# Performance work log

Measured on AMD Instinct MI355X. Metric: run time of the kernel, lower is better.

Reference implementation:

```python
import jax, jax.numpy as jnp
import numpy as np

HID = 64

def _rnn_layer(x, W_ih, W_hh, b_ih, b_hh):
    # x: [B, T, F]; PyTorch RNN step: h_t = tanh(x_t @ W_ih.T + b_ih + h_{t-1} @ W_hh.T + b_hh)
    # Precompute the input projection for all timesteps as one big GEMM.
    x_proj = jnp.einsum('btf,hf->bth', x, W_ih) + b_ih  # [B, T, H]
    B = x.shape[0]
    h0 = jnp.zeros((B, HID), x.dtype)

    def step(h, xt):
        h = jnp.tanh(xt + h @ W_hh.T + b_hh)
        return h, h

    _, hs = jax.lax.scan(step, h0, jnp.swapaxes(x_proj, 0, 1))  # hs: [T, B, H]
    return jnp.swapaxes(hs, 0, 1)  # [B, T, H]


def setup_inputs() -> dict:
    key = jax.random.key(0)
    ks = jax.random.split(key, 20)
    B, T, F = 4096, 128, 14
    s_in = 1.0 / np.sqrt(HID)  # PyTorch RNN init scale
    d = {
        'x': jax.random.normal(ks[0], (B, T, F), jnp.float32),
        'W_ih0': jax.random.normal(ks[1], (HID, F), jnp.float32) * s_in,
        'W_hh0': jax.random.normal(ks[2], (HID, HID), jnp.float32) * s_in,
        'b_ih0': jax.random.normal(ks[3], (HID,), jnp.float32) * s_in,
        'b_hh0': jax.random.normal(ks[4], (HID,), jnp.float32) * s_in,
        'W_ih1': jax.random.normal(ks[5], (HID, HID), jnp.float32) * s_in,
        'W_hh1': jax.random.normal(ks[6], (HID, HID), jnp.float32) * s_in,
        'b_ih1': jax.random.normal(ks[7], (HID,), jnp.float32) * s_in,
        'b_hh1': jax.random.normal(ks[8], (HID,), jnp.float32) * s_in,
        'W_ih2': jax.random.normal(ks[9], (HID, HID), jnp.float32) * s_in,
        'W_hh2': jax.random.normal(ks[10], (HID, HID), jnp.float32) * s_in,
        'b_ih2': jax.random.normal(ks[11], (HID,), jnp.float32) * s_in,
        'b_hh2': jax.random.normal(ks[12], (HID,), jnp.float32) * s_in,
        'fc1_w': jax.random.normal(ks[13], (32, HID), jnp.float32) * s_in,
        'fc1_b': jax.random.normal(ks[14], (32,), jnp.float32) * s_in,
        'fc2_w': jax.random.normal(ks[15], (1, 32), jnp.float32) * (1.0 / np.sqrt(32)),
        'fc2_b': jax.random.normal(ks[16], (1,), jnp.float32) * (1.0 / np.sqrt(32)),
    }
    return d


def reference(x, W_ih0, W_hh0, b_ih0, b_hh0, W_ih1, W_hh1, b_ih1, b_hh1,
              W_ih2, W_hh2, b_ih2, b_hh2, fc1_w, fc1_b, fc2_w, fc2_b):
    h = _rnn_layer(x, W_ih0, W_hh0, b_ih0, b_hh0)
    h = _rnn_layer(h, W_ih1, W_hh1, b_ih1, b_hh1)
    h = _rnn_layer(h, W_ih2, W_hh2, b_ih2, b_hh2)
    last = h[:, -1, :]                       # [B, H]
    y = jax.nn.relu(last @ fc1_w.T + fc1_b)  # [B, 32]
    return y @ fc2_w.T + fc2_b               # [B, 1]
```

## Files before the change

### kernel.cpp

```cpp
#include <hip/hip_runtime.h>

typedef short  s16x8 __attribute__((ext_vector_type(8)));
typedef float  f32x4 __attribute__((ext_vector_type(4)));
typedef float  f32x2 __attribute__((ext_vector_type(2)));
typedef unsigned int u32;
typedef unsigned int u32x4 __attribute__((ext_vector_type(4)));
typedef unsigned short u16;

#define DEVI static __device__ __forceinline__

#if __has_builtin(__builtin_amdgcn_exp2f)
#define EXP2(v) __builtin_amdgcn_exp2f(v)
#else
#define EXP2(v) exp2f(v)
#endif

constexpr int T_  = 128;
constexpr int F_  = 14;
constexpr int H_  = 64;
constexpr int BPB = 16;
constexpr int K_  = 8;
constexpr int NCH = T_ / K_;

DEVI u16 f2bf(float f) {
  u32 u = __builtin_bit_cast(u32, f);
  u += 0x7fffu + ((u >> 16) & 1u);
  return (u16)(u >> 16);
}
DEVI u16 f2bfF(float f) {
  u32 u = __builtin_bit_cast(u32, f);
  return (u16)((u + 0x8000u) >> 16);
}
DEVI u32 pkbf(float a, float b) {
  u32 ua = __builtin_bit_cast(u32, a) + 0x8000u;
  u32 ub = __builtin_bit_cast(u32, b) + 0x8000u;
  return (ua >> 16) | (ub & 0xffff0000u);
}
DEVI s16x8 packfrag(const f32x4& a, const f32x4& b) {
  u32x4 p;
  p[0] = pkbf(a[0], a[1]); p[1] = pkbf(a[2], a[3]);
  p[2] = pkbf(b[0], b[1]); p[3] = pkbf(b[2], b[3]);
  return __builtin_bit_cast(s16x8, p);
}
DEVI float tanhfast(float x) {
  float e = EXP2(x * -2.8853900817779268f);
  float r = __builtin_amdgcn_rcpf(1.0f + e);
  return __builtin_fmaf(2.0f, r, -1.0f);
}
DEVI f32x4 tanh4(const f32x4& v) {
  f32x4 r;
  r[0] = tanhfast(v[0]); r[1] = tanhfast(v[1]);
  r[2] = tanhfast(v[2]); r[3] = tanhfast(v[3]);
  return r;
}
DEVI f32x4 MFMA(s16x8 a, s16x8 b, f32x4 c) {
  return __builtin_amdgcn_mfma_f32_16x16x32_bf16(a, b, c, 0, 0, 0);
}
DEVI s16x8 ldrow8(const float* p) {
  const f32x4 a = ((const f32x4*)p)[0];
  const f32x4 b = ((const f32x4*)p)[1];
  s16x8 r;
  r[0] = (short)f2bf(a[0]); r[1] = (short)f2bf(a[1]);
  r[2] = (short)f2bf(a[2]); r[3] = (short)f2bf(a[3]);
  r[4] = (short)f2bf(b[0]); r[5] = (short)f2bf(b[1]);
  r[6] = (short)f2bf(b[2]); r[7] = (short)f2bf(b[3]);
  return r;
}

__global__ __launch_bounds__(192, 1) void rnn_ck(
    const float* __restrict__ x,
    const float* __restrict__ Wih0, const float* __restrict__ Whh0,
    const float* __restrict__ bih0, const float* __restrict__ bhh0,
    const float* __restrict__ Wih1, const float* __restrict__ Whh1,
    const float* __restrict__ bih1, const float* __restrict__ bhh1,
    const float* __restrict__ Wih2, const float* __restrict__ Whh2,
    const float* __restrict__ bih2, const float* __restrict__ bhh2,
    const float* __restrict__ fc1w, const float* __restrict__ fc1b,
    const float* __restrict__ fc2w, const float* __restrict__ fc2b,
    float* __restrict__ out)
{
  __shared__ __align__(16) u32x4 hf[2][2][K_][2][64];

  const int tid  = threadIdx.x;
  const int w    = tid >> 6;
  const int lane = tid & 63;
  const int g    = lane >> 4;
  const int m    = lane & 15;
  const int b0   = blockIdx.x * BPB;

  f32x4 z4; z4[0] = 0.f; z4[1] = 0.f; z4[2] = 0.f; z4[3] = 0.f;

  s16x8 Ax[4], Ai[4][2], Ah[4][2];
  f32x4 bc[4];
  {
    const float* Wi = Wih1; const float* Wh = Whh0;
    const float* bi = bih0; const float* bh = bhh0;
    if (w == 1)      { Wi = Wih1; Wh = Whh1; bi = bih1; bh = bhh1; }
    else if (w == 2) { Wi = Wih2; Wh = Whh2; bi = bih2; bh = bhh2; }
    #pragma unroll
    for (int n = 0; n < 4; n++) {
      const int Lr = 32 * (n & 1) + 8 * (m >> 2) + 4 * (n >> 1) + (m & 3);
      if (w == 0) {
        s16x8 r;
        #pragma unroll
        for (int j2 = 0; j2 < 8; j2++) {
          const int kk = 8 * g + j2;
          r[j2] = (kk < F_) ? (short)f2bf(Wih0[Lr * F_ + kk]) : (short)0;
        }
        Ax[n] = r;
        Ai[n][0] = r; Ai[n][1] = r;
      } else {
        #pragma unroll
        for (int kt = 0; kt < 2; kt++)
          Ai[n][kt] = ldrow8(Wi + Lr * H_ + 32 * kt + 8 * g);
        Ax[n] = Ai[n][0];
      }
      #pragma unroll
      for (int kt = 0; kt < 2; kt++)
        Ah[n][kt] = ldrow8(Wh + Lr * H_ + 32 * kt + 8 * g);
      const int Lb = 32 * (n & 1) + 8 * g + 4 * (n >> 1);
      bc[n] = *(const f32x4*)(bi + Lb) + *(const f32x4*)(bh + Lb);
    }
  }

  s16x8 F[2];
  {
    s16x8 z;
    #pragma unroll
    for (int i = 0; i < 8; i++) z[i] = 0;
    F[0] = z; F[1] = z;
  }
  f32x4 h2v[4];
  #pragma unroll
  for (int n = 0; n < 4; n++) h2v[n] = z4;

  const float* xrow = x + (size_t)(b0 + m) * T_ * F_;
  auto ldraw = [&](int t, f32x4& ra, f32x4& rb) {
    const float* p = xrow + t * F_;
    if (g == 0) {
      f32x2 p0 = *(const f32x2*)(p),     p1 = *(const f32x2*)(p + 2);
      f32x2 p2 = *(const f32x2*)(p + 4), p3 = *(const f32x2*)(p + 6);
      ra[0] = p0[0]; ra[1] = p0[1]; ra[2] = p1[0]; ra[3] = p1[1];
      rb[0] = p2[0]; rb[1] = p2[1]; rb[2] = p3[0]; rb[3] = p3[1];
    } else if (g == 1) {
      f32x2 p4 = *(const f32x2*)(p + 8), p5 = *(const f32x2*)(p + 10);
      f32x2 p6 = *(const f32x2*)(p + 12);
      ra[0] = p4[0]; ra[1] = p4[1]; ra[2] = p5[0]; ra[3] = p5[1];
      rb[0] = p6[0]; rb[1] = p6[1]; rb[2] = 0.f;   rb[3] = 0.f;
    } else {
      ra = z4; rb = z4;
    }
  };
  auto cvtraw = [&](const f32x4& ra, const f32x4& rb) -> s16x8 {
    s16x8 r;
    r[0] = (short)f2bfF(ra[0]); r[1] = (short)f2bfF(ra[1]);
    r[2] = (short)f2bfF(ra[2]); r[3] = (short)f2bfF(ra[3]);
    r[4] = (short)f2bfF(rb[0]); r[5] = (short)f2bfF(rb[1]);
    r[6] = (short)f2bfF(rb[2]); r[7] = (short)f2bfF(rb[3]);
    return r;
  };

  s16x8 cur[K_];
  f32x4 nra[K_], nrb[K_];
  if (w == 0) {
    #pragma unroll
    for (int k = 0; k < K_; k++) { ldraw(k, nra[k], nrb[k]); }
    #pragma unroll
    for (int k = 0; k < K_; k++) cur[k] = cvtraw(nra[k], nrb[k]);
  }

  #pragma unroll 1
  for (int e = 0; e < NCH + 2; e++) {
    const int c  = e - w;
    const int wb = e & 1, rb = wb ^ 1;

    if (w == 0) {
      int cn = e + 1; if (cn > NCH - 1) cn = NCH - 1;
      #pragma unroll
      for (int k = 0; k < K_; k++) ldraw(cn * K_ + k, nra[k], nrb[k]);
    }

    if (c >= 0 && c < NCH) {
      #pragma unroll
      for (int k = 0; k < K_; k++) {
        s16x8 Fp0, Fp1;
        if (w == 0) {
          Fp0 = cur[k]; Fp1 = cur[k];
        } else if (w == 1) {
          Fp0 = __builtin_bit_cast(s16x8, hf[rb][0][k][0][lane]);
          Fp1 = __builtin_bit_cast(s16x8, hf[rb][0][k][1][lane]);
        } else {
          Fp0 = __builtin_bit_cast(s16x8, hf[rb][1][k][0][lane]);
          Fp1 = __builtin_bit_cast(s16x8, hf[rb][1][k][1][lane]);
        }
        f32x4 p[4], q[4], hv[4];
        #pragma unroll
        for (int n = 0; n < 4; n++) p[n] = MFMA(Ah[n][0], F[0], bc[n]);
        #pragma unroll
        for (int n = 0; n < 4; n++) p[n] = MFMA(Ah[n][1], F[1], p[n]);
        if (w == 0) {
          #pragma unroll
          for (int n = 0; n < 4; n++) q[n] = MFMA(Ax[n], Fp0, z4);
        } else {
          #pragma unroll
          for (int n = 0; n < 4; n++) q[n] = MFMA(Ai[n][0], Fp0, z4);
          #pragma unroll
          for (int n = 0; n < 4; n++) q[n] = MFMA(Ai[n][1], Fp1, q[n]);
        }
        #pragma unroll
        for (int n = 0; n < 4; n++) hv[n] = tanh4(p[n] + q[n]);
        F[0] = packfrag(hv[0], hv[2]);
        F[1] = packfrag(hv[1], hv[3]);
        if (w < 2) {
          hf[wb][w][k][0][lane] = __builtin_bit_cast(u32x4, F[0]);
          hf[wb][w][k][1][lane] = __builtin_bit_cast(u32x4, F[1]);
        } else if (c == NCH - 1 && k == K_ - 1) {
          #pragma unroll
          for (int n = 0; n < 4; n++) h2v[n] = hv[n];
        }
      }
    }

    if (w == 0) {
      #pragma unroll
      for (int k = 0; k < K_; k++) cur[k] = cvtraw(nra[k], nrb[k]);
    }
    __syncthreads();
  }

  float (*h2l)[68] = (float (*)[68])&hf[0][0][0][0][0];
  if (w == 2) {
    #pragma unroll
    for (int n = 0; n < 4; n++) {
      const int Lb = 32 * (n & 1) + 8 * g + 4 * (n >> 1);
      *(f32x4*)&h2l[m][Lb] = h2v[n];
    }
  }
  __syncthreads();

  if (w == 0) {
    float hr[64];
    #pragma unroll
    for (int q = 0; q < 16; q++) {
      f32x4 v = *(const f32x4*)&h2l[m][4 * q];
      hr[4 * q + 0] = v[0]; hr[4 * q + 1] = v[1];
      hr[4 * q + 2] = v[2]; hr[4 * q + 3] = v[3];
    }
    float acc2 = 0.f;
    #pragma unroll
    for (int jj = 0; jj < 8; jj++) {
      const int jf = 8 * g + jj;
      float s = fc1b[jf];
      const f32x4* wp = (const f32x4*)(fc1w + jf * H_);
      #pragma unroll
      for (int kq = 0; kq < 16; kq++) {
        f32x4 wv = wp[kq];
        s += hr[4 * kq + 0] * wv[0] + hr[4 * kq + 1] * wv[1]
           + hr[4 * kq + 2] * wv[2] + hr[4 * kq + 3] * wv[3];
      }
      s = fmaxf(s, 0.f);
      acc2 += s * fc2w[jf];
    }
    acc2 += __shfl_xor(acc2, 16, 64);
    acc2 += __shfl_xor(acc2, 32, 64);
    if (lane < 16) out[b0 + m] = acc2 + fc2b[0];
  }
}

extern "C" void kernel_launch(void* const* d_in, const int* in_sizes, int n_in,
                              void* d_out, int out_size, void* d_ws, size_t ws_size,
                              hipStream_t stream) {
  const float* x    = (const float*)d_in[0];
  const float* Wih0 = (const float*)d_in[1];
  const float* Whh0 = (const float*)d_in[2];
  const float* bih0 = (const float*)d_in[3];
  const float* bhh0 = (const float*)d_in[4];
  const float* Wih1 = (const float*)d_in[5];
  const float* Whh1 = (const float*)d_in[6];
  const float* bih1 = (const float*)d_in[7];
  const float* bhh1 = (const float*)d_in[8];
  const float* Wih2 = (const float*)d_in[9];
  const float* Whh2 = (const float*)d_in[10];
  const float* bih2 = (const float*)d_in[11];
  const float* bhh2 = (const float*)d_in[12];
  const float* fc1w = (const float*)d_in[13];
  const float* fc1b = (const float*)d_in[14];
  const float* fc2w = (const float*)d_in[15];
  const float* fc2b = (const float*)d_in[16];

  rnn_ck<<<dim3(4096 / BPB), dim3(192), 0, stream>>>(
      x, Wih0, Whh0, bih0, bhh0, Wih1, Whh1, bih1, bhh1,
      Wih2, Whh2, bih2, bhh2, fc1w, fc1b, fc2w, fc2b, (float*)d_out);
}
```

Before: 191.8 us.

## Software-pipeline input projection MFMAs and split x prefetch into half-chunks

Restructures the per-timestep loop so the input-projection MFMAs for step k+1 are issued during step k, taking them off the serial recurrence chain. The two recurrent MFMA halves are computed into independent accumulators and summed afterwards, which shortens the dependent MFMA chain. Layer-0 x prefetch is split into two groups of four timesteps interleaved within the chunk, reducing live registers compared with holding eight raw rows. The cost is extra register pressure from the qc/qn buffers and more complex scheduling.

```diff
diff --git a/kernel.cpp b/kernel.cpp
--- a/kernel.cpp
+++ b/kernel.cpp
@@ -67,7 +67,7 @@
   return r;
 }
 
-__global__ __launch_bounds__(192, 1) void rnn_ck(
+__global__ __launch_bounds__(192, 1) void rnn_sp(
     const float* __restrict__ x,
     const float* __restrict__ Wih0, const float* __restrict__ Whh0,
     const float* __restrict__ bih0, const float* __restrict__ bhh0,
@@ -161,54 +161,81 @@
   };
 
   s16x8 cur[K_];
-  f32x4 nra[K_], nrb[K_];
+  f32x4 ra4[4], rb4[4];
   if (w == 0) {
     #pragma unroll
-    for (int k = 0; k < K_; k++) { ldraw(k, nra[k], nrb[k]); }
-    #pragma unroll
-    for (int k = 0; k < K_; k++) cur[k] = cvtraw(nra[k], nrb[k]);
+    for (int k = 0; k < 4; k++) ldraw(k, ra4[k], rb4[k]);
+    #pragma unroll
+    for (int k = 0; k < 4; k++) cur[k] = cvtraw(ra4[k], rb4[k]);
+    #pragma unroll
+    for (int k = 0; k < 4; k++) ldraw(4 + k, ra4[k], rb4[k]);
+    #pragma unroll
+    for (int k = 0; k < 4; k++) cur[4 + k] = cvtraw(ra4[k], rb4[k]);
+    #pragma unroll
+    for (int k = 0; k < 4; k++) ldraw(K_ + k, ra4[k], rb4[k]);
   }
 
   #pragma unroll 1
   for (int e = 0; e < NCH + 2; e++) {
     const int c  = e - w;
-    const int wb = e & 1, rb = wb ^ 1;
-
-    if (w == 0) {
-      int cn = e + 1; if (cn > NCH - 1) cn = NCH - 1;
-      #pragma unroll
-      for (int k = 0; k < K_; k++) ldraw(cn * K_ + k, nra[k], nrb[k]);
-    }
+    const int wb = e & 1, rbuf = wb ^ 1;
 
     if (c >= 0 && c < NCH) {
+      const int cn = (c + 1 < NCH) ? c + 1 : NCH - 1;
+
+      s16x8 Fpc0, Fpc1, Fpn0, Fpn1;
+      if (w == 1) {
+        Fpc0 = __builtin_bit_cast(s16x8, hf[rbuf][0][0][0][lane]);
+        Fpc1 = __builtin_bit_cast(s16x8, hf[rbuf][0][0][1][lane]);
+      } else if (w == 2) {
+        Fpc0 = __builtin_bit_cast(s16x8, hf[rbuf][1][0][0][lane]);
+        Fpc1 = __builtin_bit_cast(s16x8, hf[rbuf][1][0][1][lane]);
+      } else {
+        Fpc0 = cur[0]; Fpc1 = cur[0];
+      }
+      f32x4 qc[4], qn[4];
+      if (w == 0) {
+        #pragma unroll
+        for (int n = 0; n < 4; n++) qc[n] = MFMA(Ax[n], Fpc0, z4);
+      } else {
+        #pragma unroll
+        for (int n = 0; n < 4; n++) qc[n] = MFMA(Ai[n][0], Fpc0, z4);
+        #pragma unroll
+        for (int n = 0; n < 4; n++) qc[n] = MFMA(Ai[n][1], Fpc1, qc[n]);
+      }
+
       #pragma unroll
       for (int k = 0; k < K_; k++) {
-        s16x8 Fp0, Fp1;
-        if (w == 0) {
-          Fp0 = cur[k]; Fp1 = cur[k];
-        } else if (w == 1) {
-          Fp0 = __builtin_bit_cast(s16x8, hf[rb][0][k][0][lane]);
-          Fp1 = __builtin_bit_cast(s16x8, hf[rb][0][k][1][lane]);
-        } else {
-          Fp0 = __builtin_bit_cast(s16x8, hf[rb][1][k][0][lane]);
-          Fp1 = __builtin_bit_cast(s16x8, hf[rb][1][k][1][lane]);
+        f32x4 pA[4], pB[4];
+        #pragma unroll
+        for (int n = 0; n < 4; n++) pA[n] = MFMA(Ah[n][0], F[0], bc[n]);
+        #pragma unroll
+        for (int n = 0; n < 4; n++) pB[n] = MFMA(Ah[n][1], F[1], z4);
+
+        if (k + 1 < K_) {
+          if (w == 1) {
+            Fpn0 = __builtin_bit_cast(s16x8, hf[rbuf][0][k + 1][0][lane]);
+            Fpn1 = __builtin_bit_cast(s16x8, hf[rbuf][0][k + 1][1][lane]);
+          } else if (w == 2) {
+            Fpn0 = __builtin_bit_cast(s16x8, hf[rbuf][1][k + 1][0][lane]);
+            Fpn1 = __builtin_bit_cast(s16x8, hf[rbuf][1][k + 1][1][lane]);
+          } else {
+            Fpn0 = cur[k + 1]; Fpn1 = cur[k + 1];
+          }
+          if (w == 0) {
+            #pragma unroll
+            for (int n = 0; n < 4; n++) qn[n] = MFMA(Ax[n], Fpn0, z4);
+          } else {
+            #pragma unroll
+            for (int n = 0; n < 4; n++) qn[n] = MFMA(Ai[n][0], Fpn0, z4);
+            #pragma unroll
+            for (int n = 0; n < 4; n++) qn[n] = MFMA(Ai[n][1], Fpn1, qn[n]);
+          }
         }
-        f32x4 p[4], q[4], hv[4];
-        #pragma unroll
-        for (int n = 0; n < 4; n++) p[n] = MFMA(Ah[n][0], F[0], bc[n]);
-        #pragma unroll
-        for (int n = 0; n < 4; n++) p[n] = MFMA(Ah[n][1], F[1], p[n]);
-        if (w == 0) {
-          #pragma unroll
-          for (int n = 0; n < 4; n++) q[n] = MFMA(Ax[n], Fp0, z4);
-        } else {
-          #pragma unroll
-          for (int n = 0; n < 4; n++) q[n] = MFMA(Ai[n][0], Fp0, z4);
-          #pragma unroll
-          for (int n = 0; n < 4; n++) q[n] = MFMA(Ai[n][1], Fp1, q[n]);
-        }
-        #pragma unroll
-        for (int n = 0; n < 4; n++) hv[n] = tanh4(p[n] + q[n]);
+
+        f32x4 hv[4];
+        #pragma unroll
+        for (int n = 0; n < 4; n++) hv[n] = tanh4(pA[n] + pB[n] + qc[n]);
         F[0] = packfrag(hv[0], hv[2]);
         F[1] = packfrag(hv[1], hv[3]);
         if (w < 2) {
@@ -218,12 +245,23 @@
           #pragma unroll
           for (int n = 0; n < 4; n++) h2v[n] = hv[n];
         }
-      }
-    }
-
-    if (w == 0) {
-      #pragma unroll
-      for (int k = 0; k < K_; k++) cur[k] = cvtraw(nra[k], nrb[k]);
+        #pragma unroll
+        for (int n = 0; n < 4; n++) qc[n] = qn[n];
+
+        if (w == 0 && k == 3) {
+          #pragma unroll
+          for (int j = 0; j < 4; j++) cur[j] = cvtraw(ra4[j], rb4[j]);
+          #pragma unroll
+          for (int j = 0; j < 4; j++) ldraw(cn * K_ + 4 + j, ra4[j], rb4[j]);
+        }
+      }
+      if (w == 0) {
+        const int c2 = (c + 2 < NCH) ? c + 2 : NCH - 1;
+        #pragma unroll
+        for (int j = 0; j < 4; j++) cur[4 + j] = cvtraw(ra4[j], rb4[j]);
+        #pragma unroll
+        for (int j = 0; j < 4; j++) ldraw(c2 * K_ + j, ra4[j], rb4[j]);
+      }
     }
     __syncthreads();
   }
@@ -288,7 +326,7 @@
   const float* fc2w = (const float*)d_in[15];
   const float* fc2b = (const float*)d_in[16];
 
-  rnn_ck<<<dim3(4096 / BPB), dim3(192), 0, stream>>>(
+  rnn_sp<<<dim3(4096 / BPB), dim3(192), 0, stream>>>(
       x, Wih0, Whh0, bih0, bhh0, Wih1, Whh1, bih1, bhh1,
       Wih2, Whh2, bih2, bhh2, fc1w, fc1b, fc2w, fc2b, (float*)d_out);
 }
```

Result: slower. 205.9 us (+7.3%).
